# Performance work log

Hardware: AMD Instinct MI355X
Metric: run time of the kernel (lower is better)

The kernel has to match this reference:

```python
import jax, jax.numpy as jnp
import numpy as np
from functools import partial

B, S = 64, 256
DC, DB = 100, 100           # char / bichar embed dims
VC, VB = 10000, 200000      # vocab sizes
D_IN = (DC + DB) * 2        # 400
D_RNN = 200                 # liner output / LSTM input
H = 256                     # LSTM hidden


def setup_inputs() -> dict:
    key = jax.random.key(0)
    ks = jax.random.split(key, 20)
    s = 0.05
    return {
        "char_features": jax.random.randint(ks[0], (B, S), 0, VC),
        "bichar_left": jax.random.randint(ks[1], (B, S), 0, VB),
        "bichar_right": jax.random.randint(ks[2], (B, S), 0, VB),
        "static_char": jax.random.randint(ks[3], (B, S), 0, VC),
        "static_bichar_left": jax.random.randint(ks[4], (B, S), 0, VB),
        "static_bichar_right": jax.random.randint(ks[5], (B, S), 0, VB),
        "char_emb": jax.random.normal(ks[6], (VC, DC), jnp.float32) * s,
        "bichar_emb": jax.random.normal(ks[7], (VB, DB), jnp.float32) * s,
        "static_char_emb": jax.random.normal(ks[8], (VC, DC), jnp.float32) * s,
        "static_bichar_emb": jax.random.normal(ks[9], (VB, DB), jnp.float32) * s,
        "W_lin": jax.random.normal(ks[10], (D_RNN, D_IN), jnp.float32) * s,
        "b_lin": jnp.zeros((D_RNN,), jnp.float32),
        "Wih_l": jax.random.normal(ks[11], (4 * H, D_RNN), jnp.float32) * s,
        "Whh_l": jax.random.normal(ks[12], (4 * H, H), jnp.float32) * s,
        "bih_l": jnp.zeros((4 * H,), jnp.float32),
        "bhh_l": jnp.zeros((4 * H,), jnp.float32),
        "Wih_r": jax.random.normal(ks[13], (4 * H, D_RNN), jnp.float32) * s,
        "Whh_r": jax.random.normal(ks[14], (4 * H, H), jnp.float32) * s,
        "bih_r": jnp.zeros((4 * H,), jnp.float32),
        "bhh_r": jnp.zeros((4 * H,), jnp.float32),
    }


def _lstm_scan(xs, Wih, Whh, bih, bhh, reverse):
    # xs: [S, B, D_RNN] -> hs: [S, B, H], ordered by original time index
    b = bih + bhh

    def step(carry, x):
        h, c = carry
        gates = x @ Wih.T + h @ Whh.T + b           # [B, 4H]
        i, f, g, o = jnp.split(gates, 4, axis=-1)    # torch LSTMCell gate order
        i, f, o = jax.nn.sigmoid(i), jax.nn.sigmoid(f), jax.nn.sigmoid(o)
        g = jnp.tanh(g)
        c = f * c + i * g
        h = o * jnp.tanh(c)
        return (h, c), h

    init = (jnp.zeros((xs.shape[1], H), xs.dtype), jnp.zeros((xs.shape[1], H), xs.dtype))
    _, hs = jax.lax.scan(step, init, xs, reverse=reverse)
    return hs


def reference(char_features, bichar_left, bichar_right, static_char,
              static_bichar_left, static_bichar_right,
              char_emb, bichar_emb, static_char_emb, static_bichar_emb,
              W_lin, b_lin, Wih_l, Whh_l, bih_l, bhh_l,
              Wih_r, Whh_r, bih_r, bhh_r):
    ch = char_emb[char_features]                       # [B,S,DC]
    sch = static_char_emb[static_char]                 # [B,S,DC]
    bl = bichar_emb[bichar_left]                       # [B,S,DB]
    br = bichar_emb[bichar_right]
    sbl = static_bichar_emb[static_bichar_left]
    sbr = static_bichar_emb[static_bichar_right]

    left = jnp.concatenate([ch, sch, bl, sbl], axis=2)   # [B,S,400]
    right = jnp.concatenate([ch, sch, br, sbr], axis=2)

    left_in = jnp.tanh(left @ W_lin.T + b_lin).transpose(1, 0, 2)    # [S,B,D_RNN]
    right_in = jnp.tanh(right @ W_lin.T + b_lin).transpose(1, 0, 2)

    hs_l = _lstm_scan(left_in, Wih_l, Whh_l, bih_l, bhh_l, reverse=False)  # [S,B,H]
    hs_r = _lstm_scan(right_in, Wih_r, Whh_r, bih_r, bhh_r, reverse=True)  # [S,B,H]

    out = jnp.concatenate([hs_l, hs_r], axis=2).transpose(1, 0, 2)  # [B,S,2H]
    return out
```

## Files before the change

kernel.cpp:

```cpp
#include <hip/hip_runtime.h>
#include <math.h>

#define BB 64
#define SS 256
#define D_IN 400
#define D_RNN 200
#define HID 256
#define G4 1024

#define OFF_WTLIN 0
#define OFF_WTIH  (OFF_WTLIN + 400*200)
#define OFF_WPACK (OFF_WTIH + 2*200*1024)
#define OFF_X     (OFF_WPACK + 2*1024*256/2)
#define OFF_GX    (OFF_X + 2*64*256*200)

typedef _Float16 half2_t __attribute__((ext_vector_type(2)));

__device__ __forceinline__ half2_t u2h(unsigned u) {
    union { unsigned u; half2_t h; } x; x.u = u; return x.h;
}

__device__ __forceinline__ float dot2acc(unsigned hu, unsigned wu, float acc) {
#if __has_builtin(__builtin_amdgcn_fdot2)
    return __builtin_amdgcn_fdot2(u2h(hu), u2h(wu), acc, false);
#else
    half2_t h = u2h(hu), w = u2h(wu);
    acc = fmaf((float)h.x, (float)w.x, acc);
    acc = fmaf((float)h.y, (float)w.y, acc);
    return acc;
#endif
}

__device__ __forceinline__ unsigned packf16(float a, float b) {
    union { _Float16 h[2]; unsigned u; } x;
    x.h[0] = (_Float16)a; x.h[1] = (_Float16)b;
    return x.u;
}

__device__ __forceinline__ float sigm_f(float x) {
    return 1.0f / (1.0f + __expf(-x));
}
__device__ __forceinline__ float tanh_f(float x) {
    return 2.0f / (1.0f + __expf(-2.0f * x)) - 1.0f;
}

__global__ void kt_wlin(const float* __restrict__ W, float* __restrict__ Wt) {
    int id = blockIdx.x * 256 + threadIdx.x;
    if (id >= D_RNN * D_IN) return;
    int j = id / D_IN, k = id % D_IN;
    Wt[k * D_RNN + j] = W[id];
}

__global__ void kt_wih16(const float* __restrict__ Wl, const float* __restrict__ Wr,
                         unsigned* __restrict__ Wt16) {
    int id = blockIdx.x * 256 + threadIdx.x;
    if (id >= 2 * G4 * 100) return;
    int dir = id / (G4 * 100);
    int rem = id % (G4 * 100);
    int j = rem / 100, kk = rem % 100;
    const float* src = dir ? Wr : Wl;
    Wt16[(dir * 100 + kk) * G4 + j] = packf16(src[j * D_RNN + 2 * kk],
                                              src[j * D_RNN + 2 * kk + 1]);
}

__global__ void kt_wpack(const float* __restrict__ Wl, const float* __restrict__ Wr,
                         _Float16* __restrict__ Wp) {
    int id = blockIdx.x * 256 + threadIdx.x;
    if (id >= 2 * G4 * HID) return;
    int dir = id / (G4 * HID);
    int rem = id % (G4 * HID);
    int r = rem / HID, k = rem % HID;
    const float* src = dir ? Wr : Wl;
    Wp[(((size_t)dir * 32 + (k >> 3)) * G4 + r) * 8 + (k & 7)] = (_Float16)src[rem];
}

__launch_bounds__(512)
__global__ void k_embed_linear(const int* __restrict__ ci, const int* __restrict__ bli,
                               const int* __restrict__ bri, const int* __restrict__ sci,
                               const int* __restrict__ sbli, const int* __restrict__ sbri,
                               const float* __restrict__ ce, const float* __restrict__ be,
                               const float* __restrict__ sce, const float* __restrict__ sbe,
                               const float* __restrict__ Wt, const float* __restrict__ blin,
                               float* __restrict__ xout) {
    __shared__ __align__(16) float vec[16][2][D_IN];
    __shared__ int idx[16][6];
    int tid = threadIdx.x;
    int g0 = blockIdx.x * 16;

    if (tid < 96) {
        int tt = tid / 6, w = tid % 6;
        int g = g0 + tt;
        const int* arr = (w == 0) ? ci : (w == 1) ? sci : (w == 2) ? bli
                         : (w == 3) ? bri : (w == 4) ? sbli : sbri;
        idx[tt][w] = arr[g];
    }
    __syncthreads();

    for (int v = tid; v < 16 * D_IN; v += 512) {
        int tt = v / D_IN, p = v % D_IN;
        float lv, rv;
        if (p < 100)      { float e = ce[idx[tt][0] * 100 + p];          lv = rv = e; }
        else if (p < 200) { float e = sce[idx[tt][1] * 100 + (p - 100)]; lv = rv = e; }
        else if (p < 300) { int q = p - 200;
                            lv = be[idx[tt][2] * 100 + q];
                            rv = be[idx[tt][3] * 100 + q]; }
        else              { int q = p - 300;
                            lv = sbe[idx[tt][4] * 100 + q];
                            rv = sbe[idx[tt][5] * 100 + q]; }
        vec[tt][0][p] = lv;
        vec[tt][1][p] = rv;
    }
    __syncthreads();

    if (tid < 400) {
        int side = tid / 200, j = tid % 200;
        float acc[16];
        #pragma unroll
        for (int t = 0; t < 16; t++) acc[t] = 0.0f;

        for (int k4 = 0; k4 < D_IN / 4; k4++) {
            float w0 = Wt[(4 * k4 + 0) * D_RNN + j];
            float w1 = Wt[(4 * k4 + 1) * D_RNN + j];
            float w2 = Wt[(4 * k4 + 2) * D_RNN + j];
            float w3 = Wt[(4 * k4 + 3) * D_RNN + j];
            #pragma unroll
            for (int t = 0; t < 16; t++) {
                float4 xv = *(const float4*)&vec[t][side][4 * k4];
                acc[t] += xv.x * w0 + xv.y * w1 + xv.z * w2 + xv.w * w3;
            }
        }
        float bias = blin[j];
        #pragma unroll
        for (int t = 0; t < 16; t++) {
            int g = g0 + t;
            int b = g >> 8, s = g & 255;
            xout[((side * BB + b) * SS + s) * D_RNN + j] = tanh_f(acc[t] + bias);
        }
    }
}

__launch_bounds__(512)
__global__ void k_gatex(const float* __restrict__ x, const unsigned* __restrict__ Wt16,
                        const float* __restrict__ bihl, const float* __restrict__ bhhl,
                        const float* __restrict__ bihr, const float* __restrict__ bhhr,
                        float* __restrict__ gx) {
    __shared__ __align__(16) unsigned xT16[100][40];
    int tid = threadIdx.x;
    int id = blockIdx.x;
    int dir = id >> 9;
    int rem = id & 511;
    int b = rem >> 3;
    int s0 = (rem & 7) * 32;

    const float2* xb2 = reinterpret_cast<const float2*>(
        x + ((dir * BB + b) * SS + s0) * D_RNN);
    for (int v = tid; v < 32 * 100; v += 512) {
        int tok = v / 100, kk = v % 100;
        float2 p = xb2[tok * 100 + kk];
        xT16[kk][tok] = packf16(p.x, p.y);
    }
    __syncthreads();

    const unsigned* Wp = Wt16 + dir * 100 * G4;
    int j0 = tid, j1 = tid + 512;
    float acc0[32], acc1[32];
    #pragma unroll
    for (int t = 0; t < 32; t++) { acc0[t] = 0.0f; acc1[t] = 0.0f; }

    for (int kk = 0; kk < 100; kk++) {
        unsigned w0 = Wp[kk * G4 + j0];
        unsigned w1 = Wp[kk * G4 + j1];
        #pragma unroll
        for (int m = 0; m < 8; m++) {
            uint4 xx = *(const uint4*)&xT16[kk][4 * m];
            acc0[4 * m + 0] = dot2acc(xx.x, w0, acc0[4 * m + 0]);
            acc0[4 * m + 1] = dot2acc(xx.y, w0, acc0[4 * m + 1]);
            acc0[4 * m + 2] = dot2acc(xx.z, w0, acc0[4 * m + 2]);
            acc0[4 * m + 3] = dot2acc(xx.w, w0, acc0[4 * m + 3]);
            acc1[4 * m + 0] = dot2acc(xx.x, w1, acc1[4 * m + 0]);
            acc1[4 * m + 1] = dot2acc(xx.y, w1, acc1[4 * m + 1]);
            acc1[4 * m + 2] = dot2acc(xx.z, w1, acc1[4 * m + 2]);
            acc1[4 * m + 3] = dot2acc(xx.w, w1, acc1[4 * m + 3]);
        }
    }

    float bs0, bs1;
    if (dir) { bs0 = bihr[j0] + bhhr[j0]; bs1 = bihr[j1] + bhhr[j1]; }
    else     { bs0 = bihl[j0] + bhhl[j0]; bs1 = bihl[j1] + bhhl[j1]; }

    float* gbase = gx + ((dir * BB + b) * SS + s0) * G4;
    #pragma unroll
    for (int t = 0; t < 32; t++) {
        gbase[t * G4 + j0] = acc0[t] + bs0;
        gbase[t * G4 + j1] = acc1[t] + bs1;
    }
}

__global__ void
__attribute__((amdgpu_flat_work_group_size(512, 512), amdgpu_waves_per_eu(2, 2)))
k_lstm(const _Float16* __restrict__ wpack, const float* __restrict__ gx,
       float* __restrict__ out) {
    __shared__ __align__(16) uint4 wlds[16][512];
    __shared__ __align__(16) float4 exv[256];
    __shared__ __align__(16) unsigned hbits[2][128];

    int t = threadIdx.x;
    int c = t & 255, kh = t >> 8;
    int bid = blockIdx.x;
    int dir = bid >> 6, b = bid & 63;

    const uint4* wp = reinterpret_cast<const uint4*>(wpack) + (size_t)dir * 32 * G4;
    uint4 wreg[4][12];
    #pragma unroll
    for (int g = 0; g < 4; g++)
        #pragma unroll
        for (int i = 0; i < 12; i++)
            wreg[g][i] = wp[(kh * 16 + i) * G4 + g * 256 + c];
    #pragma unroll
    for (int g = 0; g < 4; g++)
        #pragma unroll
        for (int i = 0; i < 12; i++)
            asm volatile("" : "+v"(wreg[g][i].x), "+v"(wreg[g][i].y),
                              "+v"(wreg[g][i].z), "+v"(wreg[g][i].w));
    #pragma unroll
    for (int g = 0; g < 4; g++)
        #pragma unroll
        for (int i2 = 0; i2 < 4; i2++)
            wlds[g * 4 + i2][t] = wp[(kh * 16 + 12 + i2) * G4 + g * 256 + c];

    const float* gxp = gx + (size_t)(dir * BB + b) * SS * G4;
    float* outp = out + (size_t)b * SS * (2 * HID) + dir * HID + c;

    if (t < 128) { hbits[0][t] = 0u; }
    float cst = 0.0f;
    __syncthreads();

    int ts = dir ? (SS - 1) : 0;
    int dstep = dir ? -1 : 1;
    float gxc[4];
    if (kh == 0) {
        const float* g0p = gxp + (size_t)ts * G4;
        #pragma unroll
        for (int g = 0; g < 4; g++) gxc[g] = g0p[g * 256 + c];
    }

    for (int s = 0; s < SS; s++) {
        float ngx[4] = {0.f, 0.f, 0.f, 0.f};
        if (kh == 0 && s < SS - 1) {
            const float* gn = gxp + (size_t)(ts + dstep) * G4;
            #pragma unroll
            for (int g = 0; g < 4; g++) ngx[g] = gn[g * 256 + c];
        }

        const uint4* h4 = reinterpret_cast<const uint4*>(hbits[s & 1]);
        float a0, a1, a2, a3;
        if (kh == 0) { a0 = gxc[0]; a1 = gxc[1]; a2 = gxc[2]; a3 = gxc[3]; }
        else         { a0 = a1 = a2 = a3 = 0.0f; }

        #pragma unroll
        for (int i = 0; i < 12; i++) {
            uint4 hh = h4[kh * 16 + i];
            a0 = dot2acc(hh.x, wreg[0][i].x, a0); a0 = dot2acc(hh.y, wreg[0][i].y, a0);
            a0 = dot2acc(hh.z, wreg[0][i].z, a0); a0 = dot2acc(hh.w, wreg[0][i].w, a0);
            a1 = dot2acc(hh.x, wreg[1][i].x, a1); a1 = dot2acc(hh.y, wreg[1][i].y, a1);
            a1 = dot2acc(hh.z, wreg[1][i].z, a1); a1 = dot2acc(hh.w, wreg[1][i].w, a1);
            a2 = dot2acc(hh.x, wreg[2][i].x, a2); a2 = dot2acc(hh.y, wreg[2][i].y, a2);
            a2 = dot2acc(hh.z, wreg[2][i].z, a2); a2 = dot2acc(hh.w, wreg[2][i].w, a2);
            a3 = dot2acc(hh.x, wreg[3][i].x, a3); a3 = dot2acc(hh.y, wreg[3][i].y, a3);
            a3 = dot2acc(hh.z, wreg[3][i].z, a3); a3 = dot2acc(hh.w, wreg[3][i].w, a3);
        }
        #pragma unroll
        for (int i2 = 0; i2 < 4; i2++) {
            uint4 hh = h4[kh * 16 + 12 + i2];
            uint4 v0 = wlds[0 * 4 + i2][t];
            uint4 v1 = wlds[1 * 4 + i2][t];
            uint4 v2 = wlds[2 * 4 + i2][t];
            uint4 v3 = wlds[3 * 4 + i2][t];
            a0 = dot2acc(hh.x, v0.x, a0); a0 = dot2acc(hh.y, v0.y, a0);
            a0 = dot2acc(hh.z, v0.z, a0); a0 = dot2acc(hh.w, v0.w, a0);
            a1 = dot2acc(hh.x, v1.x, a1); a1 = dot2acc(hh.y, v1.y, a1);
            a1 = dot2acc(hh.z, v1.z, a1); a1 = dot2acc(hh.w, v1.w, a1);
            a2 = dot2acc(hh.x, v2.x, a2); a2 = dot2acc(hh.y, v2.y, a2);
            a2 = dot2acc(hh.z, v2.z, a2); a2 = dot2acc(hh.w, v2.w, a2);
            a3 = dot2acc(hh.x, v3.x, a3); a3 = dot2acc(hh.y, v3.y, a3);
            a3 = dot2acc(hh.z, v3.z, a3); a3 = dot2acc(hh.w, v3.w, a3);
        }

        if (kh == 1) exv[c] = make_float4(a0, a1, a2, a3);
        __syncthreads();

        if (kh == 0) {
            float4 p = exv[c];
            float ig = sigm_f(a0 + p.x);
            float fg = sigm_f(a1 + p.y);
            float gg = tanh_f(a2 + p.z);
            float og = sigm_f(a3 + p.w);
            cst = fg * cst + ig * gg;
            float hv = og * tanh_f(cst);
            outp[(size_t)ts * (2 * HID)] = hv;
            reinterpret_cast<unsigned short*>(hbits[(s + 1) & 1])[c] =
                __builtin_bit_cast(unsigned short, (_Float16)hv);
        }
        __syncthreads();

        if (kh == 0) {
            #pragma unroll
            for (int g = 0; g < 4; g++) gxc[g] = ngx[g];
        }
        ts += dstep;
    }
}

extern "C" void kernel_launch(void* const* d_in, const int* in_sizes, int n_in,
                              void* d_out, int out_size, void* d_ws, size_t ws_size,
                              hipStream_t stream) {
    const int* char_features      = (const int*)d_in[0];
    const int* bichar_left        = (const int*)d_in[1];
    const int* bichar_right       = (const int*)d_in[2];
    const int* static_char        = (const int*)d_in[3];
    const int* static_bichar_left = (const int*)d_in[4];
    const int* static_bichar_right= (const int*)d_in[5];
    const float* char_emb         = (const float*)d_in[6];
    const float* bichar_emb       = (const float*)d_in[7];
    const float* static_char_emb  = (const float*)d_in[8];
    const float* static_bichar_emb= (const float*)d_in[9];
    const float* W_lin            = (const float*)d_in[10];
    const float* b_lin            = (const float*)d_in[11];
    const float* Wih_l            = (const float*)d_in[12];
    const float* Whh_l            = (const float*)d_in[13];
    const float* bih_l            = (const float*)d_in[14];
    const float* bhh_l            = (const float*)d_in[15];
    const float* Wih_r            = (const float*)d_in[16];
    const float* Whh_r            = (const float*)d_in[17];
    const float* bih_r            = (const float*)d_in[18];
    const float* bhh_r            = (const float*)d_in[19];

    float* ws    = (float*)d_ws;
    float* wtlin = ws + OFF_WTLIN;
    unsigned* wtih16 = (unsigned*)(ws + OFF_WTIH);
    _Float16* wpack = (_Float16*)(ws + OFF_WPACK);
    float* xbuf  = ws + OFF_X;
    float* gxbuf = ws + OFF_GX;
    float* out   = (float*)d_out;

    kt_wlin<<<(D_RNN * D_IN + 255) / 256, 256, 0, stream>>>(W_lin, wtlin);
    kt_wih16<<<(2 * G4 * 100 + 255) / 256, 256, 0, stream>>>(Wih_l, Wih_r, wtih16);
    kt_wpack<<<(2 * G4 * HID + 255) / 256, 256, 0, stream>>>(Whh_l, Whh_r, wpack);

    k_embed_linear<<<(BB * SS) / 16, 512, 0, stream>>>(
        char_features, bichar_left, bichar_right, static_char,
        static_bichar_left, static_bichar_right,
        char_emb, bichar_emb, static_char_emb, static_bichar_emb,
        wtlin, b_lin, xbuf);

    k_gatex<<<(2 * BB * SS) / 32, 512, 0, stream>>>(
        xbuf, wtih16, bih_l, bhh_l, bih_r, bhh_r, gxbuf);

    k_lstm<<<2 * BB, 512, 0, stream>>>(wpack, gxbuf, out);
}
```

Baseline: 713.4 us.

## Split each LSTM sequence across two workgroups exchanging partial gates via global mailbox

The recurrent LSTM kernel now splits each sequence's hidden-state K dimension across two 256-thread workgroups (256 blocks total) instead of one 512-thread block. All Whh weights stay in VGPRs and AGPRs, which removes the LDS weight reads. Each block computes partial gate sums for all 1024 gates and writes half of them to a global mailbox for its sibling. The pair then synchronises every timestep with release/acquire flags. This spreads the work over more CUs, but it adds a global-memory handshake and spin-wait to every step of the serial recurrence, and it relies on both blocks of a pair being resident at the same time.

```diff
diff --git a/kernel.cpp b/kernel.cpp
--- a/kernel.cpp
+++ b/kernel.cpp
@@ -13,6 +13,8 @@
 #define OFF_WPACK (OFF_WTIH + 2*200*1024)
 #define OFF_X     (OFF_WPACK + 2*1024*256/2)
 #define OFF_GX    (OFF_X + 2*64*256*200)
+#define OFF_MAIL  OFF_X
+#define OFF_FLAG  (OFF_X + 400000)
 
 typedef _Float16 half2_t __attribute__((ext_vector_type(2)));
 
@@ -72,6 +74,11 @@
     int r = rem / HID, k = rem % HID;
     const float* src = dir ? Wr : Wl;
     Wp[(((size_t)dir * 32 + (k >> 3)) * G4 + r) * 8 + (k & 7)] = (_Float16)src[rem];
+}
+
+__global__ void kf_reset(unsigned* __restrict__ flags) {
+    int id = blockIdx.x * 1024 + threadIdx.x;
+    if (id < 256 * 32) flags[id] = 0u;
 }
 
 __launch_bounds__(512)
@@ -197,116 +204,127 @@
 }
 
 __global__ void
-__attribute__((amdgpu_flat_work_group_size(512, 512), amdgpu_waves_per_eu(2, 2)))
+__attribute__((amdgpu_flat_work_group_size(256, 256), amdgpu_waves_per_eu(1, 1)))
 k_lstm(const _Float16* __restrict__ wpack, const float* __restrict__ gx,
-       float* __restrict__ out) {
-    __shared__ __align__(16) uint4 wlds[16][512];
-    __shared__ __align__(16) float4 exv[256];
-    __shared__ __align__(16) unsigned hbits[2][128];
+       float* __restrict__ out, float* __restrict__ mail, unsigned* __restrict__ flags) {
+    __shared__ unsigned hlds[2][64];
 
     int t = threadIdx.x;
-    int c = t & 255, kh = t >> 8;
     int bid = blockIdx.x;
-    int dir = bid >> 6, b = bid & 63;
+    int seq = bid & 127, kh = bid >> 7;
+    int dir = seq >> 6, b = seq & 63;
+    bool keeper = ((t >> 7) == kh);
+    int tloc = t - kh * 128;
+    int ownf = (seq * 2 + kh) * 32;
+    int sibf = (seq * 2 + (1 - kh)) * 32;
 
     const uint4* wp = reinterpret_cast<const uint4*>(wpack) + (size_t)dir * 32 * G4;
-    uint4 wreg[4][12];
-    #pragma unroll
-    for (int g = 0; g < 4; g++)
-        #pragma unroll
-        for (int i = 0; i < 12; i++)
-            wreg[g][i] = wp[(kh * 16 + i) * G4 + g * 256 + c];
-    #pragma unroll
-    for (int g = 0; g < 4; g++)
-        #pragma unroll
-        for (int i = 0; i < 12; i++)
-            asm volatile("" : "+v"(wreg[g][i].x), "+v"(wreg[g][i].y),
-                              "+v"(wreg[g][i].z), "+v"(wreg[g][i].w));
-    #pragma unroll
-    for (int g = 0; g < 4; g++)
-        #pragma unroll
-        for (int i2 = 0; i2 < 4; i2++)
-            wlds[g * 4 + i2][t] = wp[(kh * 16 + 12 + i2) * G4 + g * 256 + c];
+    uint4 w0[16], w1[16], w2[16], w3[16];
+    #pragma unroll
+    for (int i = 0; i < 16; i++) {
+        w0[i] = wp[(kh * 16 + i) * G4 + 0 * 256 + t];
+        w1[i] = wp[(kh * 16 + i) * G4 + 1 * 256 + t];
+        w2[i] = wp[(kh * 16 + i) * G4 + 2 * 256 + t];
+        w3[i] = wp[(kh * 16 + i) * G4 + 3 * 256 + t];
+    }
+    #pragma unroll
+    for (int i = 0; i < 12; i++) {
+        asm volatile("" : "+v"(w0[i].x), "+v"(w0[i].y), "+v"(w0[i].z), "+v"(w0[i].w));
+        asm volatile("" : "+v"(w1[i].x), "+v"(w1[i].y), "+v"(w1[i].z), "+v"(w1[i].w));
+        asm volatile("" : "+v"(w2[i].x), "+v"(w2[i].y), "+v"(w2[i].z), "+v"(w2[i].w));
+        asm volatile("" : "+v"(w3[i].x), "+v"(w3[i].y), "+v"(w3[i].z), "+v"(w3[i].w));
+    }
+    #pragma unroll
+    for (int i = 12; i < 16; i++) {
+        asm volatile("" : "+a"(w0[i].x), "+a"(w0[i].y), "+a"(w0[i].z), "+a"(w0[i].w));
+        asm volatile("" : "+a"(w1[i].x), "+a"(w1[i].y), "+a"(w1[i].z), "+a"(w1[i].w));
+        asm volatile("" : "+a"(w2[i].x), "+a"(w2[i].y), "+a"(w2[i].z), "+a"(w2[i].w));
+        asm volatile("" : "+a"(w3[i].x), "+a"(w3[i].y), "+a"(w3[i].z), "+a"(w3[i].w));
+    }
 
     const float* gxp = gx + (size_t)(dir * BB + b) * SS * G4;
-    float* outp = out + (size_t)b * SS * (2 * HID) + dir * HID + c;
-
-    if (t < 128) { hbits[0][t] = 0u; }
+
+    if (t < 128) reinterpret_cast<unsigned*>(hlds)[t] = 0u;
     float cst = 0.0f;
     __syncthreads();
 
     int ts = dir ? (SS - 1) : 0;
     int dstep = dir ? -1 : 1;
-    float gxc[4];
-    if (kh == 0) {
+    float gxc[4] = {0.f, 0.f, 0.f, 0.f};
+    if (keeper) {
         const float* g0p = gxp + (size_t)ts * G4;
         #pragma unroll
-        for (int g = 0; g < 4; g++) gxc[g] = g0p[g * 256 + c];
+        for (int g = 0; g < 4; g++) gxc[g] = g0p[g * 256 + t];
     }
 
     for (int s = 0; s < SS; s++) {
+        int par = s & 1;
+
+        const uint4* hl = reinterpret_cast<const uint4*>(hlds[par]);
+        float a0 = 0.f, a1 = 0.f, a2 = 0.f, a3 = 0.f;
+        #pragma unroll
+        for (int i = 0; i < 16; i++) {
+            uint4 hh = hl[i];
+            a0 = dot2acc(hh.x, w0[i].x, a0); a0 = dot2acc(hh.y, w0[i].y, a0);
+            a0 = dot2acc(hh.z, w0[i].z, a0); a0 = dot2acc(hh.w, w0[i].w, a0);
+            a1 = dot2acc(hh.x, w1[i].x, a1); a1 = dot2acc(hh.y, w1[i].y, a1);
+            a1 = dot2acc(hh.z, w1[i].z, a1); a1 = dot2acc(hh.w, w1[i].w, a1);
+            a2 = dot2acc(hh.x, w2[i].x, a2); a2 = dot2acc(hh.y, w2[i].y, a2);
+            a2 = dot2acc(hh.z, w2[i].z, a2); a2 = dot2acc(hh.w, w2[i].w, a2);
+            a3 = dot2acc(hh.x, w3[i].x, a3); a3 = dot2acc(hh.y, w3[i].y, a3);
+            a3 = dot2acc(hh.z, w3[i].z, a3); a3 = dot2acc(hh.w, w3[i].w, a3);
+        }
+
         float ngx[4] = {0.f, 0.f, 0.f, 0.f};
-        if (kh == 0 && s < SS - 1) {
+        if (keeper && s < SS - 1) {
             const float* gn = gxp + (size_t)(ts + dstep) * G4;
             #pragma unroll
-            for (int g = 0; g < 4; g++) ngx[g] = gn[g * 256 + c];
-        }
-
-        const uint4* h4 = reinterpret_cast<const uint4*>(hbits[s & 1]);
-        float a0, a1, a2, a3;
-        if (kh == 0) { a0 = gxc[0]; a1 = gxc[1]; a2 = gxc[2]; a3 = gxc[3]; }
-        else         { a0 = a1 = a2 = a3 = 0.0f; }
-
-        #pragma unroll
-        for (int i = 0; i < 12; i++) {
-            uint4 hh = h4[kh * 16 + i];
-            a0 = dot2acc(hh.x, wreg[0][i].x, a0); a0 = dot2acc(hh.y, wreg[0][i].y, a0);
-            a0 = dot2acc(hh.z, wreg[0][i].z, a0); a0 = dot2acc(hh.w, wreg[0][i].w, a0);
-            a1 = dot2acc(hh.x, wreg[1][i].x, a1); a1 = dot2acc(hh.y, wreg[1][i].y, a1);
-            a1 = dot2acc(hh.z, wreg[1][i].z, a1); a1 = dot2acc(hh.w, wreg[1][i].w, a1);
-            a2 = dot2acc(hh.x, wreg[2][i].x, a2); a2 = dot2acc(hh.y, wreg[2][i].y, a2);
-            a2 = dot2acc(hh.z, wreg[2][i].z, a2); a2 = dot2acc(hh.w, wreg[2][i].w, a2);
-            a3 = dot2acc(hh.x, wreg[3][i].x, a3); a3 = dot2acc(hh.y, wreg[3][i].y, a3);
-            a3 = dot2acc(hh.z, wreg[3][i].z, a3); a3 = dot2acc(hh.w, wreg[3][i].w, a3);
-        }
-        #pragma unroll
-        for (int i2 = 0; i2 < 4; i2++) {
-            uint4 hh = h4[kh * 16 + 12 + i2];
-            uint4 v0 = wlds[0 * 4 + i2][t];
-            uint4 v1 = wlds[1 * 4 + i2][t];
-            uint4 v2 = wlds[2 * 4 + i2][t];
-            uint4 v3 = wlds[3 * 4 + i2][t];
-            a0 = dot2acc(hh.x, v0.x, a0); a0 = dot2acc(hh.y, v0.y, a0);
-            a0 = dot2acc(hh.z, v0.z, a0); a0 = dot2acc(hh.w, v0.w, a0);
-            a1 = dot2acc(hh.x, v1.x, a1); a1 = dot2acc(hh.y, v1.y, a1);
-            a1 = dot2acc(hh.z, v1.z, a1); a1 = dot2acc(hh.w, v1.w, a1);
-            a2 = dot2acc(hh.x, v2.x, a2); a2 = dot2acc(hh.y, v2.y, a2);
-            a2 = dot2acc(hh.z, v2.z, a2); a2 = dot2acc(hh.w, v2.w, a2);
-            a3 = dot2acc(hh.x, v3.x, a3); a3 = dot2acc(hh.y, v3.y, a3);
-            a3 = dot2acc(hh.z, v3.z, a3); a3 = dot2acc(hh.w, v3.w, a3);
-        }
-
-        if (kh == 1) exv[c] = make_float4(a0, a1, a2, a3);
+            for (int g = 0; g < 4; g++) ngx[g] = gn[g * 256 + t];
+        }
+
+        if (!keeper) {
+            int mi = ((seq * 2 + (1 - kh)) * 2 + par) * 128 + (t - (1 - kh) * 128);
+            reinterpret_cast<float4*>(mail)[mi] = make_float4(a0, a1, a2, a3);
+        }
         __syncthreads();
 
-        if (kh == 0) {
-            float4 p = exv[c];
-            float ig = sigm_f(a0 + p.x);
-            float fg = sigm_f(a1 + p.y);
-            float gg = tanh_f(a2 + p.z);
-            float og = sigm_f(a3 + p.w);
+        if (t == 0) {
+            __hip_atomic_store(&flags[ownf], (unsigned)(s + 1),
+                               __ATOMIC_RELEASE, __HIP_MEMORY_SCOPE_AGENT);
+            while (__hip_atomic_load(&flags[sibf], __ATOMIC_RELAXED,
+                                     __HIP_MEMORY_SCOPE_AGENT) < (unsigned)(s + 1)) {
+                __builtin_amdgcn_s_sleep(1);
+            }
+            (void)__hip_atomic_load(&flags[sibf], __ATOMIC_ACQUIRE,
+                                    __HIP_MEMORY_SCOPE_AGENT);
+        }
+        __syncthreads();
+
+        if (keeper) {
+            int mi = ((seq * 2 + kh) * 2 + par) * 128 + tloc;
+            const unsigned* mu = reinterpret_cast<const unsigned*>(mail) + (size_t)mi * 4;
+            float p0 = __uint_as_float(__hip_atomic_load(mu + 0, __ATOMIC_RELAXED,
+                                                         __HIP_MEMORY_SCOPE_AGENT));
+            float p1 = __uint_as_float(__hip_atomic_load(mu + 1, __ATOMIC_RELAXED,
+                                                         __HIP_MEMORY_SCOPE_AGENT));
+            float p2 = __uint_as_float(__hip_atomic_load(mu + 2, __ATOMIC_RELAXED,
+                                                         __HIP_MEMORY_SCOPE_AGENT));
+            float p3 = __uint_as_float(__hip_atomic_load(mu + 3, __ATOMIC_RELAXED,
+                                                         __HIP_MEMORY_SCOPE_AGENT));
+            float ig = sigm_f(a0 + p0 + gxc[0]);
+            float fg = sigm_f(a1 + p1 + gxc[1]);
+            float gg = tanh_f(a2 + p2 + gxc[2]);
+            float og = sigm_f(a3 + p3 + gxc[3]);
             cst = fg * cst + ig * gg;
             float hv = og * tanh_f(cst);
-            outp[(size_t)ts * (2 * HID)] = hv;
-            reinterpret_cast<unsigned short*>(hbits[(s + 1) & 1])[c] =
+            out[((size_t)b * SS + ts) * (2 * HID) + dir * HID + t] = hv;
+            reinterpret_cast<unsigned short*>(hlds[par ^ 1])[tloc] =
                 __builtin_bit_cast(unsigned short, (_Float16)hv);
-        }
-        __syncthreads();
-
-        if (kh == 0) {
             #pragma unroll
             for (int g = 0; g < 4; g++) gxc[g] = ngx[g];
         }
+        __syncthreads();
+
         ts += dstep;
     }
 }
@@ -341,6 +359,8 @@
     _Float16* wpack = (_Float16*)(ws + OFF_WPACK);
     float* xbuf  = ws + OFF_X;
     float* gxbuf = ws + OFF_GX;
+    float* mail  = ws + OFF_MAIL;
+    unsigned* flags = (unsigned*)(ws + OFF_FLAG);
     float* out   = (float*)d_out;
 
     kt_wlin<<<(D_RNN * D_IN + 255) / 256, 256, 0, stream>>>(W_lin, wtlin);
@@ -356,5 +376,7 @@
     k_gatex<<<(2 * BB * SS) / 32, 512, 0, stream>>>(
         xbuf, wtih16, bih_l, bhh_l, bih_r, bhh_r, gxbuf);
 
-    k_lstm<<<2 * BB, 512, 0, stream>>>(wpack, gxbuf, out);
-}
+    kf_reset<<<8, 1024, 0, stream>>>(flags);
+
+    k_lstm<<<256, 256, 0, stream>>>(wpack, gxbuf, out, mail, flags);
+}
```

Result: slower. 2.155 ms (+202.2%).

## Restructure LSTM recurrence to 256 threads with quad-split K and DPP reduction

Applied to the files above, without the earlier changes.

The recurrent kernel now uses 256 threads per block instead of 512. Each group of 4 lanes owns 16 gate rows and splits the 256-wide hidden dimension into four K-slices, whose partial sums are combined with DPP quad reductions. Whh is repacked so most weights stay in registers (part pinned to AGPRs) and one slice sits in a swizzled LDS buffer. This removes the cross-half exchange of the old kernel and lowers per-step LDS traffic, but it adds DPP shuffles, a gate-transpose through LDS, and very high register pressure at one wave per EU.

```diff
diff --git a/kernel.cpp b/kernel.cpp
--- a/kernel.cpp
+++ b/kernel.cpp
@@ -42,6 +42,14 @@
 }
 __device__ __forceinline__ float tanh_f(float x) {
     return 2.0f / (1.0f + __expf(-2.0f * x)) - 1.0f;
+}
+
+__device__ __forceinline__ float quad_sum(float v) {
+    int i = __float_as_int(v);
+    v += __int_as_float(__builtin_amdgcn_update_dpp(0, i, 0xB1, 0xF, 0xF, true));
+    i = __float_as_int(v);
+    v += __int_as_float(__builtin_amdgcn_update_dpp(0, i, 0x4E, 0xF, 0xF, true));
+    return v;
 }
 
 __global__ void kt_wlin(const float* __restrict__ W, float* __restrict__ Wt) {
@@ -63,15 +71,21 @@
                                               src[j * D_RNN + 2 * kk + 1]);
 }
 
-__global__ void kt_wpack(const float* __restrict__ Wl, const float* __restrict__ Wr,
-                         _Float16* __restrict__ Wp) {
+__global__ void kt_wpack3(const float* __restrict__ Wl, const float* __restrict__ Wr,
+                          uint4* __restrict__ Wp) {
     int id = blockIdx.x * 256 + threadIdx.x;
-    if (id >= 2 * G4 * HID) return;
-    int dir = id / (G4 * HID);
-    int rem = id % (G4 * HID);
-    int r = rem / HID, k = rem % HID;
+    if (id >= 2 * 8 * 1024 * 4) return;
+    int ks = id & 3;
+    int r = (id >> 2) & 1023;
+    int i = (id >> 12) & 7;
+    int dir = id >> 15;
     const float* src = dir ? Wr : Wl;
-    Wp[(((size_t)dir * 32 + (k >> 3)) * G4 + r) * 8 + (k & 7)] = (_Float16)src[rem];
+    int k0 = ks * 64 + i * 8;
+    union { unsigned short h[8]; uint4 u; } o;
+    #pragma unroll
+    for (int q = 0; q < 8; q++)
+        o.h[q] = __builtin_bit_cast(unsigned short, (_Float16)src[r * HID + k0 + q]);
+    Wp[id] = o.u;
 }
 
 __launch_bounds__(512)
@@ -197,116 +211,147 @@
 }
 
 __global__ void
-__attribute__((amdgpu_flat_work_group_size(512, 512), amdgpu_waves_per_eu(2, 2)))
-k_lstm(const _Float16* __restrict__ wpack, const float* __restrict__ gx,
+__attribute__((amdgpu_flat_work_group_size(256, 256), amdgpu_waves_per_eu(1, 1)))
+k_lstm(const uint4* __restrict__ wp3, const float* __restrict__ gx,
        float* __restrict__ out) {
-    __shared__ __align__(16) uint4 wlds[16][512];
-    __shared__ __align__(16) float4 exv[256];
-    __shared__ __align__(16) unsigned hbits[2][128];
+    __shared__ __align__(16) uint4 wl[1024 * 4];
+    __shared__ __align__(16) float gates[64 * 20];
+    __shared__ __align__(16) unsigned hbuf[4 * 36];
 
     int t = threadIdx.x;
-    int c = t & 255, kh = t >> 8;
+    int rg = t >> 2, ks = t & 3;
     int bid = blockIdx.x;
     int dir = bid >> 6, b = bid & 63;
 
-    const uint4* wp = reinterpret_cast<const uint4*>(wpack) + (size_t)dir * 32 * G4;
-    uint4 wreg[4][12];
-    #pragma unroll
-    for (int g = 0; g < 4; g++)
-        #pragma unroll
-        for (int i = 0; i < 12; i++)
-            wreg[g][i] = wp[(kh * 16 + i) * G4 + g * 256 + c];
-    #pragma unroll
-    for (int g = 0; g < 4; g++)
-        #pragma unroll
-        for (int i = 0; i < 12; i++)
-            asm volatile("" : "+v"(wreg[g][i].x), "+v"(wreg[g][i].y),
-                              "+v"(wreg[g][i].z), "+v"(wreg[g][i].w));
-    #pragma unroll
-    for (int g = 0; g < 4; g++)
-        #pragma unroll
-        for (int i2 = 0; i2 < 4; i2++)
-            wlds[g * 4 + i2][t] = wp[(kh * 16 + 12 + i2) * G4 + g * 256 + c];
+    const uint4* wp = wp3 + (size_t)dir * 8 * 1024 * 4;
+    int row0 = rg * 16;
+
+    uint4 wa[4][16], wv[3][16];
+    #pragma unroll
+    for (int i = 0; i < 4; i++)
+        #pragma unroll
+        for (int j = 0; j < 16; j++)
+            wa[i][j] = wp[(i * 1024 + row0 + j) * 4 + ks];
+    #pragma unroll
+    for (int i = 0; i < 3; i++)
+        #pragma unroll
+        for (int j = 0; j < 16; j++)
+            wv[i][j] = wp[((i + 4) * 1024 + row0 + j) * 4 + ks];
+    #pragma unroll
+    for (int i = 0; i < 4; i++)
+        #pragma unroll
+        for (int j = 0; j < 16; j++)
+            asm volatile("" : "+a"(wa[i][j].x), "+a"(wa[i][j].y),
+                              "+a"(wa[i][j].z), "+a"(wa[i][j].w));
+    #pragma unroll
+    for (int i = 0; i < 3; i++)
+        #pragma unroll
+        for (int j = 0; j < 16; j++)
+            asm volatile("" : "+v"(wv[i][j].x), "+v"(wv[i][j].y),
+                              "+v"(wv[i][j].z), "+v"(wv[i][j].w));
+    int kssw = ks ^ (rg & 3);
+    #pragma unroll
+    for (int j = 0; j < 16; j++)
+        wl[(row0 + j) * 4 + kssw] = wp[(7 * 1024 + row0 + j) * 4 + ks];
+
+    if (t < 144) hbuf[t] = 0u;
 
     const float* gxp = gx + (size_t)(dir * BB + b) * SS * G4;
-    float* outp = out + (size_t)b * SS * (2 * HID) + dir * HID + c;
-
-    if (t < 128) { hbits[0][t] = 0u; }
     float cst = 0.0f;
-    __syncthreads();
-
     int ts = dir ? (SS - 1) : 0;
     int dstep = dir ? -1 : 1;
     float gxc[4];
-    if (kh == 0) {
-        const float* g0p = gxp + (size_t)ts * G4;
-        #pragma unroll
-        for (int g = 0; g < 4; g++) gxc[g] = g0p[g * 256 + c];
-    }
+    #pragma unroll
+    for (int g = 0; g < 4; g++) gxc[g] = gxp[(size_t)ts * G4 + g * 256 + t];
+    __syncthreads();
+
+    int hb = ks * 36;
+    int wlb = row0 * 4 + kssw;
+    int g0i = (0 * 16 + (t >> 4)) * 20 + (t & 15);
+    int g1i = (1 * 16 + (t >> 4)) * 20 + (t & 15);
+    int g2i = (2 * 16 + (t >> 4)) * 20 + (t & 15);
+    int g3i = (3 * 16 + (t >> 4)) * 20 + (t & 15);
+    int hwi = ((t >> 6) * 36 + ((t & 63) >> 1)) * 2 + (t & 1);
+    unsigned short* hs = reinterpret_cast<unsigned short*>(hbuf);
+    float* outp = out + (size_t)b * SS * (2 * HID) + dir * HID + t;
 
     for (int s = 0; s < SS; s++) {
-        float ngx[4] = {0.f, 0.f, 0.f, 0.f};
-        if (kh == 0 && s < SS - 1) {
-            const float* gn = gxp + (size_t)(ts + dstep) * G4;
-            #pragma unroll
-            for (int g = 0; g < 4; g++) ngx[g] = gn[g * 256 + c];
-        }
-
-        const uint4* h4 = reinterpret_cast<const uint4*>(hbits[s & 1]);
-        float a0, a1, a2, a3;
-        if (kh == 0) { a0 = gxc[0]; a1 = gxc[1]; a2 = gxc[2]; a3 = gxc[3]; }
-        else         { a0 = a1 = a2 = a3 = 0.0f; }
-
-        #pragma unroll
-        for (int i = 0; i < 12; i++) {
-            uint4 hh = h4[kh * 16 + i];
-            a0 = dot2acc(hh.x, wreg[0][i].x, a0); a0 = dot2acc(hh.y, wreg[0][i].y, a0);
-            a0 = dot2acc(hh.z, wreg[0][i].z, a0); a0 = dot2acc(hh.w, wreg[0][i].w, a0);
-            a1 = dot2acc(hh.x, wreg[1][i].x, a1); a1 = dot2acc(hh.y, wreg[1][i].y, a1);
-            a1 = dot2acc(hh.z, wreg[1][i].z, a1); a1 = dot2acc(hh.w, wreg[1][i].w, a1);
-            a2 = dot2acc(hh.x, wreg[2][i].x, a2); a2 = dot2acc(hh.y, wreg[2][i].y, a2);
-            a2 = dot2acc(hh.z, wreg[2][i].z, a2); a2 = dot2acc(hh.w, wreg[2][i].w, a2);
-            a3 = dot2acc(hh.x, wreg[3][i].x, a3); a3 = dot2acc(hh.y, wreg[3][i].y, a3);
-            a3 = dot2acc(hh.z, wreg[3][i].z, a3); a3 = dot2acc(hh.w, wreg[3][i].w, a3);
-        }
-        #pragma unroll
-        for (int i2 = 0; i2 < 4; i2++) {
-            uint4 hh = h4[kh * 16 + 12 + i2];
-            uint4 v0 = wlds[0 * 4 + i2][t];
-            uint4 v1 = wlds[1 * 4 + i2][t];
-            uint4 v2 = wlds[2 * 4 + i2][t];
-            uint4 v3 = wlds[3 * 4 + i2][t];
-            a0 = dot2acc(hh.x, v0.x, a0); a0 = dot2acc(hh.y, v0.y, a0);
-            a0 = dot2acc(hh.z, v0.z, a0); a0 = dot2acc(hh.w, v0.w, a0);
-            a1 = dot2acc(hh.x, v1.x, a1); a1 = dot2acc(hh.y, v1.y, a1);
-            a1 = dot2acc(hh.z, v1.z, a1); a1 = dot2acc(hh.w, v1.w, a1);
-            a2 = dot2acc(hh.x, v2.x, a2); a2 = dot2acc(hh.y, v2.y, a2);
-            a2 = dot2acc(hh.z, v2.z, a2); a2 = dot2acc(hh.w, v2.w, a2);
-            a3 = dot2acc(hh.x, v3.x, a3); a3 = dot2acc(hh.y, v3.y, a3);
-            a3 = dot2acc(hh.z, v3.z, a3); a3 = dot2acc(hh.w, v3.w, a3);
-        }
-
-        if (kh == 1) exv[c] = make_float4(a0, a1, a2, a3);
+        uint4 h0 = *(const uint4*)&hbuf[hb + 0];
+        uint4 h1 = *(const uint4*)&hbuf[hb + 4];
+        uint4 h2 = *(const uint4*)&hbuf[hb + 8];
+        uint4 h3 = *(const uint4*)&hbuf[hb + 12];
+
+        float acc[16];
+        #pragma unroll
+        for (int j = 0; j < 16; j++) acc[j] = 0.0f;
+
+#define DOT4(A, H, W4) \
+        A = dot2acc((H).x, (W4).x, A); A = dot2acc((H).y, (W4).y, A); \
+        A = dot2acc((H).z, (W4).z, A); A = dot2acc((H).w, (W4).w, A);
+
+        #pragma unroll
+        for (int j = 0; j < 16; j++) { DOT4(acc[j], h0, wa[0][j]); }
+        uint4 h4 = *(const uint4*)&hbuf[hb + 16];
+        uint4 h5 = *(const uint4*)&hbuf[hb + 20];
+        #pragma unroll
+        for (int j = 0; j < 16; j++) { DOT4(acc[j], h1, wa[1][j]); }
+        uint4 h6 = *(const uint4*)&hbuf[hb + 24];
+        uint4 h7 = *(const uint4*)&hbuf[hb + 28];
+        #pragma unroll
+        for (int j = 0; j < 16; j++) { DOT4(acc[j], h2, wa[2][j]); }
+        #pragma unroll
+        for (int j = 0; j < 16; j++) { DOT4(acc[j], h3, wa[3][j]); }
+        #pragma unroll
+        for (int j = 0; j < 16; j++) { DOT4(acc[j], h4, wv[0][j]); }
+        #pragma unroll
+        for (int j = 0; j < 16; j++) { DOT4(acc[j], h5, wv[1][j]); }
+        #pragma unroll
+        for (int j = 0; j < 16; j++) { DOT4(acc[j], h6, wv[2][j]); }
+
+        {
+            uint4 q0 = wl[wlb + 0],  q1 = wl[wlb + 4];
+            uint4 q2 = wl[wlb + 8],  q3 = wl[wlb + 12];
+            uint4 r0 = wl[wlb + 16], r1 = wl[wlb + 20];
+            uint4 r2 = wl[wlb + 24], r3 = wl[wlb + 28];
+            DOT4(acc[0], h7, q0); DOT4(acc[1], h7, q1);
+            DOT4(acc[2], h7, q2); DOT4(acc[3], h7, q3);
+            q0 = wl[wlb + 32]; q1 = wl[wlb + 36]; q2 = wl[wlb + 40]; q3 = wl[wlb + 44];
+            DOT4(acc[4], h7, r0); DOT4(acc[5], h7, r1);
+            DOT4(acc[6], h7, r2); DOT4(acc[7], h7, r3);
+            r0 = wl[wlb + 48]; r1 = wl[wlb + 52]; r2 = wl[wlb + 56]; r3 = wl[wlb + 60];
+            DOT4(acc[8], h7, q0);  DOT4(acc[9], h7, q1);
+            DOT4(acc[10], h7, q2); DOT4(acc[11], h7, q3);
+            DOT4(acc[12], h7, r0); DOT4(acc[13], h7, r1);
+            DOT4(acc[14], h7, r2); DOT4(acc[15], h7, r3);
+        }
+#undef DOT4
+
+        #pragma unroll
+        for (int j = 0; j < 16; j++) acc[j] = quad_sum(acc[j]);
+
+        if (ks == 0) {
+            *(float4*)&gates[rg * 20 + 0]  = make_float4(acc[0], acc[1], acc[2], acc[3]);
+            *(float4*)&gates[rg * 20 + 4]  = make_float4(acc[4], acc[5], acc[6], acc[7]);
+            *(float4*)&gates[rg * 20 + 8]  = make_float4(acc[8], acc[9], acc[10], acc[11]);
+            *(float4*)&gates[rg * 20 + 12] = make_float4(acc[12], acc[13], acc[14], acc[15]);
+        }
         __syncthreads();
 
-        if (kh == 0) {
-            float4 p = exv[c];
-            float ig = sigm_f(a0 + p.x);
-            float fg = sigm_f(a1 + p.y);
-            float gg = tanh_f(a2 + p.z);
-            float og = sigm_f(a3 + p.w);
+        {
+            float ig = sigm_f(gates[g0i] + gxc[0]);
+            float fg = sigm_f(gates[g1i] + gxc[1]);
+            float gg = tanh_f(gates[g2i] + gxc[2]);
+            float og = sigm_f(gates[g3i] + gxc[3]);
             cst = fg * cst + ig * gg;
             float hv = og * tanh_f(cst);
             outp[(size_t)ts * (2 * HID)] = hv;
-            reinterpret_cast<unsigned short*>(hbits[(s + 1) & 1])[c] =
-                __builtin_bit_cast(unsigned short, (_Float16)hv);
+            hs[hwi] = __builtin_bit_cast(unsigned short, (_Float16)hv);
+            int tn = (s < SS - 1) ? (ts + dstep) : ts;
+            #pragma unroll
+            for (int g = 0; g < 4; g++) gxc[g] = gxp[(size_t)tn * G4 + g * 256 + t];
         }
         __syncthreads();
 
-        if (kh == 0) {
-            #pragma unroll
-            for (int g = 0; g < 4; g++) gxc[g] = ngx[g];
-        }
         ts += dstep;
     }
 }
@@ -338,14 +383,14 @@
     float* ws    = (float*)d_ws;
     float* wtlin = ws + OFF_WTLIN;
     unsigned* wtih16 = (unsigned*)(ws + OFF_WTIH);
-    _Float16* wpack = (_Float16*)(ws + OFF_WPACK);
+    uint4* wp3   = (uint4*)(ws + OFF_WPACK);
     float* xbuf  = ws + OFF_X;
     float* gxbuf = ws + OFF_GX;
     float* out   = (float*)d_out;
 
     kt_wlin<<<(D_RNN * D_IN + 255) / 256, 256, 0, stream>>>(W_lin, wtlin);
     kt_wih16<<<(2 * G4 * 100 + 255) / 256, 256, 0, stream>>>(Wih_l, Wih_r, wtih16);
-    kt_wpack<<<(2 * G4 * HID + 255) / 256, 256, 0, stream>>>(Whh_l, Whh_r, wpack);
+    kt_wpack3<<<(2 * 8 * 1024 * 4) / 256, 256, 0, stream>>>(Whh_l, Whh_r, wp3);
 
     k_embed_linear<<<(BB * SS) / 16, 512, 0, stream>>>(
         char_features, bichar_left, bichar_right, static_char,
@@ -356,5 +401,5 @@
     k_gatex<<<(2 * BB * SS) / 32, 512, 0, stream>>>(
         xbuf, wtih16, bih_l, bhh_l, bih_r, bhh_r, gxbuf);
 
-    k_lstm<<<2 * BB, 512, 0, stream>>>(wpack, gxbuf, out);
-}
+    k_lstm<<<2 * BB, 256, 0, stream>>>(wp3, gxbuf, out);
+}
```

Result: slower. 924.1 us (+29.5%).
